# Optimization experiments

Hardware: AMD Instinct MI355X
Metric: run time of the kernel (lower is better)

The kernel has to match this reference:

```python
import jax, jax.numpy as jnp
import numpy as np
import math

B, C, MX, MY, MZ = 4, 64, 32, 32, 32
N_ATOM, EMB, N_HEAD = 64, 128, 8
HEAD = C // N_HEAD


def setup_inputs() -> dict:
    key = jax.random.key(0)
    ks = jax.random.split(key, 12)
    s = 0.05
    return {
        "x": jax.random.normal(ks[0], (B, C, MX, MY, MZ), jnp.float32),
        "mol_embed": jax.random.normal(ks[1], (B, N_ATOM, EMB), jnp.float32),
        "batch_nodes": jax.random.randint(ks[2], (B,), 1, N_ATOM + 1),  # >=1 valid atom
        "Wq": jax.random.normal(ks[3], (C, C), jnp.float32) * s,
        "bq": jnp.zeros((C,), jnp.float32),
        "Wk": jax.random.normal(ks[4], (C, EMB), jnp.float32) * s,
        "bk": jnp.zeros((C,), jnp.float32),
        "Wv": jax.random.normal(ks[5], (C, EMB), jnp.float32) * s,
        "bv": jnp.zeros((C,), jnp.float32),
        "Wo": jax.random.normal(ks[6], (C, C), jnp.float32) * s,
        "bo": jnp.zeros((C,), jnp.float32),
        "Wc": jax.random.normal(ks[7], (C, C, 3, 3, 3), jnp.float32) * s,
        "bc": jnp.zeros((C,), jnp.float32),
    }


def reference(x, mol_embed, batch_nodes, Wq, bq, Wk, bk, Wv, bv, Wo, bo, Wc, bc):
    b, c, mx, my, mz = x.shape
    m_voxel = mx * my * mz
    n_atom = mol_embed.shape[1]
    x_in = x

    # [b, m_voxel, c] voxel tokens
    xt = x.reshape(b, c, m_voxel).transpose(0, 2, 1)
    q = (xt @ Wq.T + bq).reshape(b, m_voxel, N_HEAD, HEAD)
    k = (mol_embed @ Wk.T + bk).reshape(b, n_atom, N_HEAD, HEAD)
    v = (mol_embed @ Wv.T + bv).reshape(b, n_atom, N_HEAD, HEAD)

    att = jnp.einsum('bqhd,bkhd->bhqk', q, k) / math.sqrt(HEAD)
    # ragged per-batch masking: atoms >= batch_nodes[i] are invalid
    valid = jnp.arange(n_atom)[None, :] < batch_nodes[:, None]  # [b, n_atom]
    att = jnp.where(valid[:, None, None, :], att, -jnp.inf)
    att = jax.nn.softmax(att, axis=-1)

    o = jnp.einsum('bhqk,bkhd->bqhd', att, v).reshape(b, m_voxel, c)
    o = jax.nn.relu(o @ Wo.T + bo)
    o = o.transpose(0, 2, 1).reshape(b, c, mx, my, mz)

    # conv3d k=3 with circular padding
    op = jnp.pad(o, ((0, 0), (0, 0), (1, 1), (1, 1), (1, 1)), mode='wrap')
    conv = jax.lax.conv_general_dilated(
        op, Wc, window_strides=(1, 1, 1), padding='VALID',
        dimension_numbers=('NCDHW', 'OIDHW', 'NCDHW'))
    conv = conv + bc[None, :, None, None, None]
    return jax.nn.relu(conv) + x_in
```

## Files before the change

kernel.cpp:

```cpp
#include <hip/hip_runtime.h>
#include <hip/hip_bf16.h>

#define B_    4
#define C_    64
#define MVOX  32768
#define NATOM 64
#define EMB_  128

typedef __attribute__((ext_vector_type(8)))  __bf16 bf16x8;
typedef __attribute__((ext_vector_type(4)))  float  f32x4;
typedef __attribute__((ext_vector_type(16))) float  f32x16;
typedef __attribute__((ext_vector_type(8)))  unsigned short ushort8;

typedef __attribute__((address_space(1))) const unsigned int gas_u32;
typedef __attribute__((address_space(3))) unsigned int las_u32;

static __device__ __forceinline__ unsigned short bf16u(float f) {
  __hip_bfloat16 h = __float2bfloat16(f);
  return *(unsigned short*)&h;
}

__global__ __launch_bounds__(256) void wprep_kernel(
    const float* __restrict__ Wc, const float* __restrict__ Wq,
    const float* __restrict__ Wo, const float* __restrict__ Wk,
    const float* __restrict__ Wv,
    __hip_bfloat16* __restrict__ Wt4, __hip_bfloat16* __restrict__ Wqb,
    __hip_bfloat16* __restrict__ Wob, __hip_bfloat16* __restrict__ Wkb,
    __hip_bfloat16* __restrict__ Wvb) {
  const int i = blockIdx.x * 256 + threadIdx.x;
  if (i < 110592) {
    const int tap = i >> 12;
    const int coh = (i >> 11) & 1;
    const int ks  = (i >> 9) & 3;
    const int l   = (i >> 3) & 63;
    const int j   = i & 7;
    const int co  = coh * 32 + (l & 31);
    const int ci  = ks * 16 + ((l >> 5) << 3) + j;
    Wt4[i] = __float2bfloat16(Wc[(co * C_ + ci) * 27 + tap]);
  } else if (i < 114688) {
    const int i2 = i - 110592;
    const int nf = (i2 >> 10) & 3;
    const int kk = (i2 >> 9) & 1;
    const int l  = (i2 >> 3) & 63;
    const int j  = i2 & 7;
    const int co = nf * 16 + (l & 15);
    const int ci = kk * 32 + ((l >> 4) << 3) + j;
    Wqb[i2] = __float2bfloat16(Wq[co * C_ + ci] * 0.3535533905932738f);
  } else if (i < 118784) {
    const int i3 = i - 114688;
    const int nf = (i3 >> 10) & 3;
    const int kk = (i3 >> 9) & 1;
    const int l  = (i3 >> 3) & 63;
    const int j  = i3 & 7;
    const int co = nf * 16 + (l & 15);
    const int ci = kk * 32 + ((l >> 4) << 3) + j;
    Wob[i3] = __float2bfloat16(Wo[co * C_ + ci]);
  } else if (i < 135168) {
    const int i4 = (i - 118784) & 8191;
    const bool is_v = (i - 118784) >= 8192;
    const int ch = i4 >> 12;
    const int kk = (i4 >> 9) & 7;
    const int l  = (i4 >> 3) & 63;
    const int j  = i4 & 7;
    const int c  = ch * 32 + (l & 31);
    const int e  = kk * 16 + ((l >> 5) << 3) + j;
    const float v = (is_v ? Wv : Wk)[c * EMB_ + e];
    (is_v ? Wvb : Wkb)[i4] = __float2bfloat16(v);
  }
}

__global__ __launch_bounds__(256) void kv_kernel(
    const float* __restrict__ mol,
    const __hip_bfloat16* __restrict__ Wkb, const float* __restrict__ bk,
    const __hip_bfloat16* __restrict__ Wvb, const float* __restrict__ bv,
    unsigned short* __restrict__ kfb, unsigned short* __restrict__ vfb) {
  __shared__ float smol[NATOM][132];
  __shared__ float res[2][NATOM][68];

  const int b    = blockIdx.x;
  const int tid  = threadIdx.x;
  const int lane = tid & 63;
  const int w    = tid >> 6;
  const int kvw  = w >> 1;
  const int ah   = w & 1;

  for (int i = tid; i < 2048; i += 256) {
    const int a = i >> 4, cb = (i & 15) * 8;
    const f32x4 v0 = *(const f32x4*)&mol[(size_t)(b * NATOM + a) * EMB_ + cb];
    const f32x4 v1 = *(const f32x4*)&mol[(size_t)(b * NATOM + a) * EMB_ + cb + 4];
    *(f32x4*)&smol[a][cb]     = v0;
    *(f32x4*)&smol[a][cb + 4] = v1;
  }
  __syncthreads();

  const __hip_bfloat16* Wb   = kvw ? Wvb : Wkb;
  const float*          bias = kvw ? bv : bk;

  f32x16 acc[2];
  #pragma unroll
  for (int ch = 0; ch < 2; ++ch)
    #pragma unroll
    for (int r = 0; r < 16; ++r) acc[ch][r] = 0.f;

  const int a = ah * 32 + (lane & 31);
  #pragma unroll
  for (int kk = 0; kk < 8; ++kk) {
    const int e0 = kk * 16 + ((lane >> 5) << 3);
    ushort8 au;
    #pragma unroll
    for (int j = 0; j < 8; ++j) au[j] = bf16u(smol[a][e0 + j]);
    const bf16x8 af = __builtin_bit_cast(bf16x8, au);
    #pragma unroll
    for (int ch = 0; ch < 2; ++ch) {
      const bf16x8 bf = *(const bf16x8*)(Wb + (((ch * 8 + kk) << 6) + lane) * 8);
      acc[ch] = __builtin_amdgcn_mfma_f32_32x32x16_bf16(af, bf, acc[ch], 0, 0, 0);
    }
  }

  #pragma unroll
  for (int ch = 0; ch < 2; ++ch) {
    const int c = ch * 32 + (lane & 31);
    const float bb = bias[c];
    #pragma unroll
    for (int r = 0; r < 16; ++r) {
      const int ar = ah * 32 + (r & 3) + 8 * (r >> 2) + 4 * (lane >> 5);
      res[kvw][ar][c] = acc[ch][r] + bb;
    }
  }
  __syncthreads();

  #pragma unroll
  for (int t = 0; t < 8; ++t) {
    const int idx = t * 256 + tid;
    const int h = idx >> 8, aa = (idx >> 6) & 3, ln = idx & 63;
    const int qd = ln >> 4, l15 = ln & 15;
    ushort8 au;
    if (qd == 0) {
      #pragma unroll
      for (int j = 0; j < 8; ++j) au[j] = bf16u(res[0][aa * 16 + l15][h * 8 + j]);
    } else {
      #pragma unroll
      for (int j = 0; j < 8; ++j) au[j] = 0;
    }
    *(ushort8*)(kfb + (size_t)(((b * 8 + h) * 4 + aa) * 64 + ln) * 8) = au;
  }
  #pragma unroll
  for (int t = 0; t < 4; ++t) {
    const int idx = t * 256 + tid;
    const int h = idx >> 7, s = (idx >> 6) & 1, ln = idx & 63;
    const int qd = ln >> 4, l15 = ln & 15;
    ushort8 au;
    #pragma unroll
    for (int j = 0; j < 8; ++j) {
      const int atom = (2 * s + (j >> 2)) * 16 + qd * 4 + (j & 3);
      au[j] = bf16u(res[1][atom][h * 8 + (l15 & 7)]);
    }
    *(ushort8*)(vfb + (size_t)(((b * 8 + h) * 2 + s) * 64 + ln) * 8) = au;
  }
}

__global__ __launch_bounds__(512, 4) void attn_kernel(
    const float* __restrict__ x,
    const unsigned short* __restrict__ kfb, const unsigned short* __restrict__ vfb,
    const int* __restrict__ batch_nodes,
    const __hip_bfloat16* __restrict__ Wqb, const float* __restrict__ bq,
    const __hip_bfloat16* __restrict__ Wob, const float* __restrict__ bo,
    __hip_bfloat16* __restrict__ omid) {
  __shared__ float buf[64 * C_];

  const int b    = blockIdx.y;
  const int m0   = blockIdx.x * 64;
  const int tid  = threadIdx.x;
  const int lane = tid & 63;
  const int w    = __builtin_amdgcn_readfirstlane(tid >> 6);
  const int h    = w;
  const int quad = lane >> 4;
  const int l15  = lane & 15;
  const int vq   = w & 3;
  const int cq   = w >> 2;

  bf16x8 kf[4], vf[2];
  #pragma unroll
  for (int a = 0; a < 4; ++a)
    kf[a] = __builtin_bit_cast(bf16x8,
        *(const ushort8*)(kfb + (size_t)(((b * 8 + h) * 4 + a) * 64 + lane) * 8));
  #pragma unroll
  for (int s = 0; s < 2; ++s)
    vf[s] = __builtin_bit_cast(bf16x8,
        *(const ushort8*)(vfb + (size_t)(((b * 8 + h) * 2 + s) * 64 + lane) * 8));

  #pragma unroll
  for (int j = 0; j < 2; ++j) {
    const int cidx = w * 2 + j;
    const int c  = cidx * 4 + (lane >> 4);
    const int v4 = (lane & 15) * 4;
    const float* gsrc = x + (size_t)(b * C_ + c) * MVOX + m0 + v4;
    __builtin_amdgcn_global_load_lds((gas_u32*)gsrc,
                                     (las_u32*)&buf[cidx * 256], 16, 0, 0);
  }
  __syncthreads();

  f32x4 qacc[2];
  {
    bf16x8 af[2];
    #pragma unroll
    for (int kk = 0; kk < 2; ++kk) {
      ushort8 au;
      #pragma unroll
      for (int j = 0; j < 8; ++j)
        au[j] = bf16u(buf[(kk * 32 + quad * 8 + j) * 64 + vq * 16 + l15]);
      af[kk] = __builtin_bit_cast(bf16x8, au);
    }
    #pragma unroll
    for (int nf2 = 0; nf2 < 2; ++nf2) {
      const int nf = cq * 2 + nf2;
      const float bqv = bq[nf * 16 + l15] * 0.3535533905932738f;
      qacc[nf2] = {bqv, bqv, bqv, bqv};
      #pragma unroll
      for (int kk = 0; kk < 2; ++kk) {
        const bf16x8 bf = *(const bf16x8*)(Wqb + (((nf * 2 + kk) << 6) + lane) * 8);
        qacc[nf2] = __builtin_amdgcn_mfma_f32_16x16x32_bf16(af[kk], bf, qacc[nf2], 0, 0, 0);
      }
    }
  }
  __syncthreads();

  unsigned short* qb = (unsigned short*)buf;
  #pragma unroll
  for (int nf2 = 0; nf2 < 2; ++nf2) {
    const int co = (cq * 2 + nf2) * 16 + l15;
    #pragma unroll
    for (int r = 0; r < 4; ++r) {
      const int vr = vq * 16 + quad * 4 + r;
      qb[vr * 64 + (((co >> 3) ^ (vr & 7)) << 3) + (co & 7)] = bf16u(qacc[nf2][r]);
    }
  }
  __syncthreads();

  const int nv = batch_nodes[b];
  unsigned short* ob = (unsigned short*)buf + 4096;

  f32x4 oacc[4];
  #pragma unroll
  for (int v = 0; v < 4; ++v)
    #pragma unroll
    for (int r = 0; r < 4; ++r) oacc[v][r] = 0.f;

  const f32x4 zero4 = {0.f, 0.f, 0.f, 0.f};
  #pragma unroll
  for (int v = 0; v < 4; ++v) {
    const int qrow = v * 16 + l15;
    const bf16x8 qf = __builtin_bit_cast(bf16x8,
        *(const ushort8*)&qb[qrow * 64 + ((h ^ (qrow & 7)) << 3)]);

    f32x4 st[4];
    #pragma unroll
    for (int a = 0; a < 4; ++a)
      st[a] = __builtin_amdgcn_mfma_f32_16x16x32_bf16(kf[a], qf, zero4, 0, 0, 0);

    float m = -1e30f;
    #pragma unroll
    for (int a = 0; a < 4; ++a)
      #pragma unroll
      for (int r = 0; r < 4; ++r) {
        const int atom = a * 16 + quad * 4 + r;
        const float val = (atom < nv) ? st[a][r] : -1e30f;
        st[a][r] = val;
        m = fmaxf(m, val);
      }
    m = fmaxf(m, __shfl_xor(m, 16, 64));
    m = fmaxf(m, __shfl_xor(m, 32, 64));
    float ssum = 0.f;
    #pragma unroll
    for (int a = 0; a < 4; ++a)
      #pragma unroll
      for (int r = 0; r < 4; ++r) {
        const float p = __expf(st[a][r] - m);
        st[a][r] = p;
        ssum += p;
      }
    ssum += __shfl_xor(ssum, 16, 64);
    ssum += __shfl_xor(ssum, 32, 64);
    const float inv = 1.f / ssum;

    #pragma unroll
    for (int s = 0; s < 2; ++s) {
      ushort8 pu;
      #pragma unroll
      for (int j = 0; j < 8; ++j)
        pu[j] = bf16u(st[2 * s + (j >> 2)][j & 3] * inv);
      const bf16x8 pa = __builtin_bit_cast(bf16x8, pu);
      oacc[v] = __builtin_amdgcn_mfma_f32_16x16x32_bf16(pa, vf[s], oacc[v], 0, 0, 0);
    }
  }

  if (l15 < 8) {
    #pragma unroll
    for (int v = 0; v < 4; ++v)
      #pragma unroll
      for (int r = 0; r < 4; ++r) {
        const int vxr = v * 16 + quad * 4 + r;
        ob[vxr * 64 + ((h ^ (vxr & 7)) << 3) + l15] = bf16u(oacc[v][r]);
      }
  }
  __syncthreads();

  {
    bf16x8 af[2];
    #pragma unroll
    for (int kk = 0; kk < 2; ++kk) {
      const int row = vq * 16 + l15;
      af[kk] = __builtin_bit_cast(bf16x8,
          *(const ushort8*)&ob[row * 64 + (((kk * 4 + quad) ^ (row & 7)) << 3)]);
    }
    f32x4 oac[2];
    #pragma unroll
    for (int nf2 = 0; nf2 < 2; ++nf2) {
      const int nf = cq * 2 + nf2;
      const float bov = bo[nf * 16 + l15];
      oac[nf2] = {bov, bov, bov, bov};
      #pragma unroll
      for (int kk = 0; kk < 2; ++kk) {
        const bf16x8 bf = *(const bf16x8*)(Wob + (((nf * 2 + kk) << 6) + lane) * 8);
        oac[nf2] = __builtin_amdgcn_mfma_f32_16x16x32_bf16(af[kk], bf, oac[nf2], 0, 0, 0);
      }
    }
    __syncthreads();
    unsigned short* osb = (unsigned short*)buf;
    #pragma unroll
    for (int nf2 = 0; nf2 < 2; ++nf2) {
      const int co = (cq * 2 + nf2) * 16 + l15;
      #pragma unroll
      for (int r = 0; r < 4; ++r) {
        const int vr = vq * 16 + quad * 4 + r;
        osb[vr * 64 + (((co >> 3) ^ (vr & 7)) << 3) + (co & 7)] =
            bf16u(fmaxf(oac[nf2][r], 0.f));
      }
    }
  }
  __syncthreads();

  *(ushort8*)(omid + (size_t)(b * MVOX + m0) * C_ + tid * 8) =
      *(const ushort8*)&((unsigned short*)buf)[tid * 8];
}

#define LOADB(dst, DX, DY, DZ)                                              \
  {                                                                         \
    const int zp_ = ((lane & 31) + (DZ) + 31) & 31;                         \
    const int sw_ = zp_ & 7;                                                \
    _Pragma("unroll")                                                       \
    for (int ks_ = 0; ks_ < 4; ++ks_) {                                     \
      const int phys_ = (ks_ * 2 + (lane >> 5)) ^ sw_;                      \
      _Pragma("unroll")                                                     \
      for (int i_ = 0; i_ < 2; ++i_) {                                      \
        const int hl_ = (lp + (DX)) * 4 + (i_ + (DY));                      \
        (dst)[i_ * 4 + ks_] =                                               \
            *(const bf16x8*)&halo[((hl_ * 32 + zp_) * 8 + phys_) * 8];      \
      }                                                                     \
    }                                                                       \
  }

#define LOADW(T2)                                                           \
  _Pragma("unroll")                                                         \
  for (int ks_ = 0; ks_ < 4; ++ks_)                                         \
    wf[(T2) % 3][ks_] =                                                     \
        *(const bf16x8*)(Wt4 + ((((T2) * 2 + coh) * 4 + ks_) << 9) + lane * 8);

#define DOMFMA(src, T)                                                      \
  _Pragma("unroll")                                                         \
  for (int ks_ = 0; ks_ < 4; ++ks_)                                         \
    _Pragma("unroll")                                                       \
    for (int i_ = 0; i_ < 2; ++i_)                                          \
      acc[i_] = __builtin_amdgcn_mfma_f32_32x32x16_bf16(                    \
          wf[(T) % 3][ks_], (src)[i_ * 4 + ks_], acc[i_], 0, 0, 0);

__global__ __launch_bounds__(256, 2) void conv_kernel(
    const __hip_bfloat16* __restrict__ omid,
    const __hip_bfloat16* __restrict__ Wt4,
    const float* __restrict__ bc,
    const float* __restrict__ xin,
    float* __restrict__ out) {
  __shared__ __hip_bfloat16 halo[512 * 64];

  const int b    = blockIdx.y;
  const int x0   = (blockIdx.x >> 4) * 2;
  const int y0   = (blockIdx.x & 15) * 2;
  const int tid  = threadIdx.x;
  const int lane = tid & 63;
  const int w    = tid >> 6;
  const int coh  = w & 1;
  const int lp   = w >> 1;

  {
    const __hip_bfloat16* src = omid + (size_t)b * MVOX * C_;
    #pragma unroll
    for (int n = 0; n < 16; ++n) {
      const int chunk = w * 16 + n;
      const int li = chunk >> 2;
      const int zb = (chunk & 3) * 8;
      const int gx = (x0 - 1 + (li >> 2)) & 31;
      const int gy = (y0 - 1 + (li & 3)) & 31;
      const __hip_bfloat16* gsrc = src + (size_t)(gx * 1024 + gy * 32 + zb) * C_ + lane * 8;
      __builtin_amdgcn_global_load_lds((gas_u32*)gsrc,
                                       (las_u32*)&halo[chunk * 512], 16, 0, 0);
    }
  }

  bf16x8 wf[3][4];
  LOADW(0);
  LOADW(1);
  __syncthreads();

  f32x16 acc[2];
  #pragma unroll
  for (int i = 0; i < 2; ++i)
    #pragma unroll
    for (int r = 0; r < 16; ++r) acc[i][r] = 0.f;

  bf16x8 bR[3][8];
  LOADB(bR[0], 0, 0, 0);
  LOADB(bR[1], 0, 0, 1);

  #pragma unroll
  for (int t = 0; t < 27; ++t) {
    const int tn = t + 2;
    if (tn < 27) {
      LOADB(bR[tn % 3], tn / 9, (tn / 3) % 3, tn % 3);
      LOADW(tn);
    }
    DOMFMA(bR[t % 3], t);
  }

  const int z = lane & 31;
  #pragma unroll
  for (int i = 0; i < 2; ++i) {
    const int gx = x0 + lp, gy = y0 + i;
    #pragma unroll
    for (int r = 0; r < 16; ++r) {
      const int co = coh * 32 + (r & 3) + 8 * (r >> 2) + 4 * (lane >> 5);
      const size_t idx = ((size_t)(b * C_ + co)) * MVOX + gx * 1024 + gy * 32 + z;
      out[idx] = fmaxf(acc[i][r] + bc[co], 0.f) + xin[idx];
    }
  }
}

extern "C" void kernel_launch(void* const* d_in, const int* in_sizes, int n_in,
                              void* d_out, int out_size, void* d_ws, size_t ws_size,
                              hipStream_t stream) {
  const float* x   = (const float*)d_in[0];
  const float* mol = (const float*)d_in[1];
  const int*   bn  = (const int*)  d_in[2];
  const float* Wq  = (const float*)d_in[3];
  const float* bq  = (const float*)d_in[4];
  const float* Wk  = (const float*)d_in[5];
  const float* bk  = (const float*)d_in[6];
  const float* Wv  = (const float*)d_in[7];
  const float* bv  = (const float*)d_in[8];
  const float* Wo  = (const float*)d_in[9];
  const float* bo  = (const float*)d_in[10];
  const float* Wc  = (const float*)d_in[11];
  const float* bc  = (const float*)d_in[12];
  float* out = (float*)d_out;

  char* ws = (char*)d_ws;
  __hip_bfloat16* omid = (__hip_bfloat16*)ws;
  __hip_bfloat16* Wt4  = (__hip_bfloat16*)(ws + 16777216);
  __hip_bfloat16* Wqb  = (__hip_bfloat16*)(ws + 16998400);
  __hip_bfloat16* Wob  = (__hip_bfloat16*)(ws + 17006592);
  __hip_bfloat16* Wkb  = (__hip_bfloat16*)(ws + 17014784);
  __hip_bfloat16* Wvb  = (__hip_bfloat16*)(ws + 17031168);
  unsigned short* kfb  = (unsigned short*)(ws + 17047552);
  unsigned short* vfb  = (unsigned short*)(ws + 17178624);

  wprep_kernel<<<dim3(528), 256, 0, stream>>>(Wc, Wq, Wo, Wk, Wv,
                                              Wt4, Wqb, Wob, Wkb, Wvb);
  kv_kernel<<<dim3(B_), 256, 0, stream>>>(mol, Wkb, bk, Wvb, bv, kfb, vfb);
  attn_kernel<<<dim3(MVOX / 64, B_), 512, 0, stream>>>(x, kfb, vfb, bn, Wqb, bq, Wob, bo, omid);
  conv_kernel<<<dim3(256, B_), 256, 0, stream>>>(omid, Wt4, bc, x, out);
}
```

Before: 83.29 us.

## Enlarge conv tile to 4x4 columns and skip masked atom tiles in attention

The conv kernel now has each block compute a 4x4 xy tile with 512 threads and a 6x6 halo, so each wave handles four y rows per weight fetch. This raises reuse of both halo data and weight fragments and shrinks the halo overhead from 4x4 per 2x2 to 6x6 per 4x4. Register buffering moves from three stages to two, with bigger accumulators. Separately, attention skips QK and PV MFMAs and softmax work for atom tiles past batch_nodes. The cost is much higher register pressure from 4 f32x16 accumulators and 32 B fragments, which may reduce occupancy or spill.

After: 90.55 us. 8.7% more time.

```diff
diff --git a/kernel.cpp b/kernel.cpp
--- a/kernel.cpp
+++ b/kernel.cpp
@@ -237,7 +237,8 @@
   }
   __syncthreads();
 
-  const int nv = batch_nodes[b];
+  const int nv     = batch_nodes[b];
+  const int natile = (nv + 15) >> 4;
   unsigned short* ob = (unsigned short*)buf + 4096;
 
   f32x4 oacc[4];
@@ -255,29 +256,37 @@
 
     f32x4 st[4];
     #pragma unroll
+    for (int a = 0; a < 4; ++a) {
+      if (a < natile)
+        st[a] = __builtin_amdgcn_mfma_f32_16x16x32_bf16(kf[a], qf, zero4, 0, 0, 0);
+      else
+        st[a] = zero4;
+    }
+
+    float m = -1e30f;
+    #pragma unroll
     for (int a = 0; a < 4; ++a)
-      st[a] = __builtin_amdgcn_mfma_f32_16x16x32_bf16(kf[a], qf, zero4, 0, 0, 0);
-
-    float m = -1e30f;
-    #pragma unroll
-    for (int a = 0; a < 4; ++a)
-      #pragma unroll
-      for (int r = 0; r < 4; ++r) {
-        const int atom = a * 16 + quad * 4 + r;
-        const float val = (atom < nv) ? st[a][r] : -1e30f;
-        st[a][r] = val;
-        m = fmaxf(m, val);
+      if (a < natile) {
+        #pragma unroll
+        for (int r = 0; r < 4; ++r) {
+          const int atom = a * 16 + quad * 4 + r;
+          const float val = (atom < nv) ? st[a][r] : -1e30f;
+          st[a][r] = val;
+          m = fmaxf(m, val);
+        }
       }
     m = fmaxf(m, __shfl_xor(m, 16, 64));
     m = fmaxf(m, __shfl_xor(m, 32, 64));
     float ssum = 0.f;
     #pragma unroll
     for (int a = 0; a < 4; ++a)
-      #pragma unroll
-      for (int r = 0; r < 4; ++r) {
-        const float p = __expf(st[a][r] - m);
-        st[a][r] = p;
-        ssum += p;
+      if (a < natile) {
+        #pragma unroll
+        for (int r = 0; r < 4; ++r) {
+          const float p = __expf(st[a][r] - m);
+          st[a][r] = p;
+          ssum += p;
+        }
       }
     ssum += __shfl_xor(ssum, 16, 64);
     ssum += __shfl_xor(ssum, 32, 64);
@@ -285,12 +294,17 @@
 
     #pragma unroll
     for (int s = 0; s < 2; ++s) {
-      ushort8 pu;
-      #pragma unroll
-      for (int j = 0; j < 8; ++j)
-        pu[j] = bf16u(st[2 * s + (j >> 2)][j & 3] * inv);
-      const bf16x8 pa = __builtin_bit_cast(bf16x8, pu);
-      oacc[v] = __builtin_amdgcn_mfma_f32_16x16x32_bf16(pa, vf[s], oacc[v], 0, 0, 0);
+      if (s * 32 < nv) {
+        ushort8 pu;
+        #pragma unroll
+        for (int j = 0; j < 8; ++j) {
+          const int tile = 2 * s + (j >> 2);
+          pu[j] = (tile < natile) ? bf16u(st[tile][j & 3] * inv)
+                                  : (unsigned short)0;
+        }
+        const bf16x8 pa = __builtin_bit_cast(bf16x8, pu);
+        oacc[v] = __builtin_amdgcn_mfma_f32_16x16x32_bf16(pa, vf[s], oacc[v], 0, 0, 0);
+      }
     }
   }
 
@@ -352,9 +366,9 @@
     for (int ks_ = 0; ks_ < 4; ++ks_) {                                     \
       const int phys_ = (ks_ * 2 + (lane >> 5)) ^ sw_;                      \
       _Pragma("unroll")                                                     \
-      for (int i_ = 0; i_ < 2; ++i_) {                                      \
-        const int hl_ = (lp + (DX)) * 4 + (i_ + (DY));                      \
-        (dst)[i_ * 4 + ks_] =                                               \
+      for (int ly_ = 0; ly_ < 4; ++ly_) {                                   \
+        const int hl_ = (lg + (DX)) * 6 + (ly_ + (DY));                     \
+        (dst)[ly_ * 4 + ks_] =                                              \
             *(const bf16x8*)&halo[((hl_ * 32 + zp_) * 8 + phys_) * 8];      \
       }                                                                     \
     }                                                                       \
@@ -363,83 +377,85 @@
 #define LOADW(T2)                                                           \
   _Pragma("unroll")                                                         \
   for (int ks_ = 0; ks_ < 4; ++ks_)                                         \
-    wf[(T2) % 3][ks_] =                                                     \
+    wf[(T2) & 1][ks_] =                                                     \
         *(const bf16x8*)(Wt4 + ((((T2) * 2 + coh) * 4 + ks_) << 9) + lane * 8);
 
 #define DOMFMA(src, T)                                                      \
   _Pragma("unroll")                                                         \
   for (int ks_ = 0; ks_ < 4; ++ks_)                                         \
     _Pragma("unroll")                                                       \
-    for (int i_ = 0; i_ < 2; ++i_)                                          \
-      acc[i_] = __builtin_amdgcn_mfma_f32_32x32x16_bf16(                    \
-          wf[(T) % 3][ks_], (src)[i_ * 4 + ks_], acc[i_], 0, 0, 0);
-
-__global__ __launch_bounds__(256, 2) void conv_kernel(
+    for (int ly_ = 0; ly_ < 4; ++ly_)                                       \
+      acc[ly_] = __builtin_amdgcn_mfma_f32_32x32x16_bf16(                   \
+          wf[(T) & 1][ks_], (src)[ly_ * 4 + ks_], acc[ly_], 0, 0, 0);
+
+__global__ __launch_bounds__(512, 2) void conv_kernel(
     const __hip_bfloat16* __restrict__ omid,
     const __hip_bfloat16* __restrict__ Wt4,
     const float* __restrict__ bc,
     const float* __restrict__ xin,
     float* __restrict__ out) {
-  __shared__ __hip_bfloat16 halo[512 * 64];
+  __shared__ __hip_bfloat16 halo[36 * 32 * 64];
 
   const int b    = blockIdx.y;
-  const int x0   = (blockIdx.x >> 4) * 2;
-  const int y0   = (blockIdx.x & 15) * 2;
+  const int x0   = (blockIdx.x >> 3) * 4;
+  const int y0   = (blockIdx.x & 7) * 4;
   const int tid  = threadIdx.x;
   const int lane = tid & 63;
   const int w    = tid >> 6;
   const int coh  = w & 1;
-  const int lp   = w >> 1;
+  const int lg   = w >> 1;
 
   {
     const __hip_bfloat16* src = omid + (size_t)b * MVOX * C_;
     #pragma unroll
-    for (int n = 0; n < 16; ++n) {
-      const int chunk = w * 16 + n;
+    for (int n = 0; n < 18; ++n) {
+      const int chunk = w * 18 + n;
       const int li = chunk >> 2;
       const int zb = (chunk & 3) * 8;
-      const int gx = (x0 - 1 + (li >> 2)) & 31;
-      const int gy = (y0 - 1 + (li & 3)) & 31;
+      const int hx = li / 6, hy = li % 6;
+      const int gx = (x0 - 1 + hx) & 31;
+      const int gy = (y0 - 1 + hy) & 31;
       const __hip_bfloat16* gsrc = src + (size_t)(gx * 1024 + gy * 32 + zb) * C_ + lane * 8;
       __builtin_amdgcn_global_load_lds((gas_u32*)gsrc,
                                        (las_u32*)&halo[chunk * 512], 16, 0, 0);
     }
   }
 
-  bf16x8 wf[3][4];
+  bf16x8 wf[2][4];
   LOADW(0);
-  LOADW(1);
-  __syncthreads();
-
-  f32x16 acc[2];
-  #pragma unroll
-  for (int i = 0; i < 2; ++i)
-    #pragma unroll
-    for (int r = 0; r < 16; ++r) acc[i][r] = 0.f;
-
-  bf16x8 bR[3][8];
-  LOADB(bR[0], 0, 0, 0);
-  LOADB(bR[1], 0, 0, 1);
+  __syncthreads();
+
+  f32x16 acc[4];
+  #pragma unroll
+  for (int ly = 0; ly < 4; ++ly)
+    #pragma unroll
+    for (int r = 0; r < 16; ++r) acc[ly][r] = 0.f;
+
+  bf16x8 bA[16], bB[16];
+  LOADB(bA, 0, 0, 0);
 
   #pragma unroll
   for (int t = 0; t < 27; ++t) {
-    const int tn = t + 2;
+    const int tn = t + 1;
     if (tn < 27) {
-      LOADB(bR[tn % 3], tn / 9, (tn / 3) % 3, tn % 3);
+      if ((t & 1) == 0) LOADB(bB, tn / 9, (tn / 3) % 3, tn % 3)
+      else              LOADB(bA, tn / 9, (tn / 3) % 3, tn % 3)
       LOADW(tn);
     }
-    DOMFMA(bR[t % 3], t);
+    if ((t & 1) == 0) DOMFMA(bA, t)
+    else              DOMFMA(bB, t)
   }
 
   const int z = lane & 31;
-  #pragma unroll
-  for (int i = 0; i < 2; ++i) {
-    const int gx = x0 + lp, gy = y0 + i;
+  const int gx = x0 + lg;
+  #pragma unroll
+  for (int ly = 0; ly < 4; ++ly) {
+    const int gy = y0 + ly;
     #pragma unroll
     for (int r = 0; r < 16; ++r) {
       const int co = coh * 32 + (r & 3) + 8 * (r >> 2) + 4 * (lane >> 5);
       const size_t idx = ((size_t)(b * C_ + co)) * MVOX + gx * 1024 + gy * 32 + z;
-      out[idx] = fmaxf(acc[i][r] + bc[co], 0.f) + xin[idx];
+      out[idx] = fmaxf(acc[ly][r] + bc[co], 0.f) + xin[idx];
     }
   }
 }
@@ -476,5 +492,5 @@
                                               Wt4, Wqb, Wob, Wkb, Wvb);
   kv_kernel<<<dim3(B_), 256, 0, stream>>>(mol, Wkb, bk, Wvb, bv, kfb, vfb);
   attn_kernel<<<dim3(MVOX / 64, B_), 512, 0, stream>>>(x, kfb, vfb, bn, Wqb, bq, Wob, bo, omid);
-  conv_kernel<<<dim3(256, B_), 256, 0, stream>>>(omid, Wt4, bc, x, out);
-}
+  conv_kernel<<<dim3(64, B_), 512, 0, stream>>>(omid, Wt4, bc, x, out);
+}
```
